# Optimization experiments

Hardware: AMD Instinct MI355X
Metric: run time of the kernel (lower is better)

Reference implementation:

```python
import jax, jax.numpy as jnp
import numpy as np

RATIO = 0.25
RADIUS = 0.2
K = 32  # PyG radius() default max_num_neighbors


def fps(pos, n_samples):
    """Farthest point sampling for one cloud. pos: [N,3] -> indices [S]."""
    d2 = jnp.sum((pos - pos[0]) ** 2, axis=-1)  # dist to first (deterministic start)
    idx0 = jnp.zeros((n_samples,), jnp.int32)

    def body(i, state):
        idx, d = state
        nxt = jnp.argmax(d).astype(jnp.int32)
        idx = idx.at[i].set(nxt)
        d = jnp.minimum(d, jnp.sum((pos - pos[nxt]) ** 2, axis=-1))
        return idx, d

    idx, _ = jax.lax.fori_loop(1, n_samples, body, (idx0, d2))
    return idx


def setup_inputs() -> dict:
    key = jax.random.key(0)
    k0, k1, k2, k3 = jax.random.split(key, 4)
    B, N, C = 16, 4096, 64
    x = jax.random.normal(k0, (B, N, C), jnp.float32)
    pos = jax.random.uniform(k1, (B, N, 3), jnp.float32)  # unit cube
    W1 = jax.random.normal(k2, (C + 3, 128), jnp.float32) / np.sqrt(C + 3).astype(np.float32)
    b1 = jnp.zeros((128,), jnp.float32)
    W2 = jax.random.normal(k3, (128, 256), jnp.float32) / np.sqrt(128).astype(np.float32)
    b2 = jnp.zeros((256,), jnp.float32)
    return {"x": x, "pos": pos, "W1": W1, "b1": b1, "W2": W2, "b2": b2}


def reference(x, pos, W1, b1, W2, b2):
    B, N, C = x.shape
    S = int(N * RATIO)
    r2 = RADIUS * RADIUS

    # --- FPS per cloud ---
    samp = jax.vmap(lambda p: fps(p, S))(pos)            # [B,S] int32
    pos_s = jnp.take_along_axis(pos, samp[..., None], axis=1)  # [B,S,3]

    # --- ball query: K nearest within radius of each centroid ---
    d2 = jnp.sum((pos_s[:, :, None, :] - pos[:, None, :, :]) ** 2, axis=-1)  # [B,S,N]
    neg = jnp.where(d2 <= r2, -d2, -jnp.inf)
    negk, nbr = jax.lax.top_k(neg, K)                    # [B,S,K]
    valid = negk > -jnp.inf                              # centroid itself (d2=0) always valid

    # --- gather -> local MLP -> max pool (PointConv with max aggregation) ---
    x_j = jax.vmap(lambda xb, nb: xb[nb])(x, nbr)        # [B,S,K,C]
    pos_j = jax.vmap(lambda pb, nb: pb[nb])(pos, nbr)    # [B,S,K,3]
    rel = pos_j - pos_s[:, :, None, :]                   # pos_j - pos_i
    h = jnp.concatenate([x_j, rel], axis=-1)             # [B,S,K,C+3]
    h = jax.nn.relu(jnp.einsum("bskc,cd->bskd", h, W1) + b1)
    h = jax.nn.relu(jnp.einsum("bskd,de->bske", h, W2) + b2)
    h = jnp.where(valid[..., None], h, -jnp.inf)
    out = jnp.max(h, axis=2)                             # [B,S,256]
    return out, pos_s
```

## Files before the change

kernel.cpp:

```cpp
#include <hip/hip_runtime.h>
#include <stdint.h>

typedef unsigned short u16;
typedef unsigned int u32;
typedef unsigned long long u64;

#define NB 16
#define NP 4096
#define NCH 64
#define NS 1024
#define NK 32
#define H1D 128
#define H2D 256
#define KP1 96
#define LDA 104
#define LDH 136
#define OUTOFF (NB * NS * H2D)

typedef __attribute__((ext_vector_type(8))) short bfrag;
typedef __attribute__((ext_vector_type(4))) float facc4;
typedef __attribute__((ext_vector_type(2))) float f32x2;

__device__ __forceinline__ u16 f2bf(float f) {
  u32 u = __float_as_uint(f);
  u += 0x7FFFu + ((u >> 16) & 1u);
  return (u16)(u >> 16);
}

__device__ __forceinline__ float dist2(float ax, float ay, float az,
                                       float bx, float by, float bz) {
#pragma clang fp contract(off)
  float dx = ax - bx, dy = ay - by, dz = az - bz;
  return dx * dx + dy * dy + dz * dz;
}

__device__ __forceinline__ f32x2 dist2v(f32x2 ax, f32x2 ay, f32x2 az,
                                        float bx, float by, float bz) {
#pragma clang fp contract(off)
  f32x2 dx = ax - bx, dy = ay - by, dz = az - bz;
  return dx * dx + dy * dy + dz * dz;
}

__device__ __forceinline__ float wave_max_f32(float v) {
  const int NI = (int)0xFF800000u;
  v = fmaxf(v, __int_as_float(__builtin_amdgcn_update_dpp(NI, __float_as_int(v), 0x111, 0xf, 0xf, false)));
  v = fmaxf(v, __int_as_float(__builtin_amdgcn_update_dpp(NI, __float_as_int(v), 0x112, 0xf, 0xf, false)));
  v = fmaxf(v, __int_as_float(__builtin_amdgcn_update_dpp(NI, __float_as_int(v), 0x114, 0xf, 0xf, false)));
  v = fmaxf(v, __int_as_float(__builtin_amdgcn_update_dpp(NI, __float_as_int(v), 0x118, 0xf, 0xf, false)));
  v = fmaxf(v, __int_as_float(__builtin_amdgcn_update_dpp(NI, __float_as_int(v), 0x142, 0xa, 0xf, false)));
  v = fmaxf(v, __int_as_float(__builtin_amdgcn_update_dpp(NI, __float_as_int(v), 0x143, 0xc, 0xf, false)));
  return __int_as_float(__builtin_amdgcn_readlane(__float_as_int(v), 63));
}

__device__ __forceinline__ u32 wave_min_u32(u32 v) {
  u32 t;
  t = (u32)__builtin_amdgcn_update_dpp(-1, (int)v, 0x111, 0xf, 0xf, false); v = t < v ? t : v;
  t = (u32)__builtin_amdgcn_update_dpp(-1, (int)v, 0x112, 0xf, 0xf, false); v = t < v ? t : v;
  t = (u32)__builtin_amdgcn_update_dpp(-1, (int)v, 0x114, 0xf, 0xf, false); v = t < v ? t : v;
  t = (u32)__builtin_amdgcn_update_dpp(-1, (int)v, 0x118, 0xf, 0xf, false); v = t < v ? t : v;
  t = (u32)__builtin_amdgcn_update_dpp(-1, (int)v, 0x142, 0xa, 0xf, false); v = t < v ? t : v;
  t = (u32)__builtin_amdgcn_update_dpp(-1, (int)v, 0x143, 0xc, 0xf, false); v = t < v ? t : v;
  return (u32)__builtin_amdgcn_readlane((int)v, 63);
}

#define QUAD_MAX_STEP(CTRL)                                                           \
  {                                                                                   \
    const u32 plo = (u32)__builtin_amdgcn_update_dpp(0, (int)klo, (CTRL), 0xf, 0xf, true); \
    const u32 phi = (u32)__builtin_amdgcn_update_dpp(0, (int)khi, (CTRL), 0xf, 0xf, true); \
    const u32 pqx = (u32)__builtin_amdgcn_update_dpp(0, (int)qxu, (CTRL), 0xf, 0xf, true); \
    const u32 pqy = (u32)__builtin_amdgcn_update_dpp(0, (int)qyu, (CTRL), 0xf, 0xf, true); \
    const u32 pqz = (u32)__builtin_amdgcn_update_dpp(0, (int)qzu, (CTRL), 0xf, 0xf, true); \
    const u64 ok = ((u64)phi << 32) | plo;                                            \
    const u64 mk = ((u64)khi << 32) | klo;                                            \
    if (ok > mk) { klo = plo; khi = phi; qxu = pqx; qyu = pqy; qzu = pqz; }           \
  }

__global__ void setup_kernel(const float* __restrict__ W1, const float* __restrict__ W2,
                             u16* __restrict__ W1T, u16* __restrict__ W2T) {
  int idx = blockIdx.x * 256 + threadIdx.x;
  if (idx < H1D * KP1) {
    int n = idx / KP1, k = idx % KP1;
    W1T[idx] = f2bf(k < 67 ? W1[k * H1D + n] : 0.f);
  } else if (idx < H1D * KP1 + H2D * H1D) {
    int j = idx - H1D * KP1;
    int n = j / H1D, k = j % H1D;
    W2T[j] = f2bf(W2[k * H2D + n]);
  }
}

__global__ __launch_bounds__(256) void fps_kernel(const float* __restrict__ pos,
                                                  int* __restrict__ samp,
                                                  float* __restrict__ pos_s) {
  __shared__ float4 plds[NP];
  __shared__ __align__(16) u32 recs[2][4][8];
  const int b = blockIdx.x;
  const int tid = threadIdx.x;
  const int lane = tid & 63, wv = tid >> 6;
  const float* pb = pos + (size_t)b * NP * 3;
  for (int k = tid; k < NP; k += 256)
    plds[k] = make_float4(pb[k * 3 + 0], pb[k * 3 + 1], pb[k * 3 + 2], 0.f);
  __syncthreads();

  f32x2 px2[8], py2[8], pz2[8], dd[8];
  const float4 q0 = plds[0];
  float bv = -1.f;
  int bj = 0;
#pragma unroll
  for (int t = 0; t < 8; ++t) {
    const float4 pA = plds[tid * 16 + 2 * t];
    const float4 pB = plds[tid * 16 + 2 * t + 1];
    px2[t] = (f32x2){pA.x, pB.x};
    py2[t] = (f32x2){pA.y, pB.y};
    pz2[t] = (f32x2){pA.z, pB.z};
    const f32x2 s = dist2v(px2[t], py2[t], pz2[t], q0.x, q0.y, q0.z);
    dd[t] = s;
    const bool c0 = s.x > bv; bv = c0 ? s.x : bv; bj = c0 ? 2 * t : bj;
    const bool c1 = s.y > bv; bv = c1 ? s.y : bv; bj = c1 ? 2 * t + 1 : bj;
  }
  if (tid == 0) {
    samp[b * NS] = 0;
    pos_s[(size_t)b * NS * 3 + 0] = q0.x;
    pos_s[(size_t)b * NS * 3 + 1] = q0.y;
    pos_s[(size_t)b * NS * 3 + 2] = q0.z;
  }

  for (int i = 1; i < NS; ++i) {
    const int gidx = tid * 16 + bj;
    const float4 cpos = plds[gidx];
    const float wmax = wave_max_f32(bv);
    const u64 mask = __ballot(bv == wmax);
    const bool winner = (bv == wmax) && ((mask & ((1ull << lane) - 1ull)) == 0ull);
    if (winner) {
      u32* rp = &recs[i & 1][wv][0];
      *(uint4*)rp = make_uint4(4095u - (u32)gidx, __float_as_uint(bv),
                               __float_as_uint(cpos.x), __float_as_uint(cpos.y));
      rp[4] = __float_as_uint(cpos.z);
    }
    __syncthreads();
    const u32* sp = &recs[i & 1][lane & 3][0];
    const uint4 rA = *(const uint4*)sp;
    u32 klo = rA.x, khi = rA.y, qxu = rA.z, qyu = rA.w, qzu = sp[4];
    QUAD_MAX_STEP(0xB1)
    QUAD_MAX_STEP(0x4E)
    const float qx = __uint_as_float(qxu);
    const float qy = __uint_as_float(qyu);
    const float qz = __uint_as_float(qzu);
    if (tid == 0) {
      samp[b * NS + i] = 4095 - (int)(klo & 0xFFFu);
      pos_s[((size_t)b * NS + i) * 3 + 0] = qx;
      pos_s[((size_t)b * NS + i) * 3 + 1] = qy;
      pos_s[((size_t)b * NS + i) * 3 + 2] = qz;
    }
    bv = -1.f; bj = 0;
#pragma unroll
    for (int t = 0; t < 8; ++t) {
      const f32x2 s = dist2v(px2[t], py2[t], pz2[t], qx, qy, qz);
      dd[t].x = fminf(dd[t].x, s.x);
      dd[t].y = fminf(dd[t].y, s.y);
      const bool c0 = dd[t].x > bv; bv = c0 ? dd[t].x : bv; bj = c0 ? 2 * t : bj;
      const bool c1 = dd[t].y > bv; bv = c1 ? dd[t].y : bv; bj = c1 ? 2 * t + 1 : bj;
    }
  }
}

__global__ __launch_bounds__(256) void ballq_kernel(const float* __restrict__ pos,
                                                    const int* __restrict__ samp,
                                                    int* __restrict__ nbr) {
  __shared__ u64 buf[4][256];
  const int lane = threadIdx.x & 63, wv = threadIdx.x >> 6;
  const int sg = blockIdx.x * 4 + wv;
  const int b = sg >> 10;
  const int nc = samp[sg];
  const float* pb = pos + (size_t)b * NP * 3;
  const float cx = pb[nc * 3 + 0], cy = pb[nc * 3 + 1], cz = pb[nc * 3 + 2];
  const float r2 = (float)(0.2 * 0.2);
  int V = 0;
  for (int c = 0; c < 64; ++c) {
    const int i = c * 64 + lane;
    const float d2v = dist2(cx, cy, cz, pb[i * 3 + 0], pb[i * 3 + 1], pb[i * 3 + 2]);
    const bool valid = d2v <= r2;
    const u64 bal = __ballot(valid);
    if (valid) {
      const int rank = __popcll(bal & ((1ull << lane) - 1ull));
      const int p = V + rank;
      if (p < 256) buf[wv][p] = ((u64)__float_as_uint(d2v) << 32) | (u32)i;
    }
    V += __popcll(bal);
  }
  if (V > 256) V = 256;
  u32 kd[4], ki[4];
#pragma unroll
  for (int t = 0; t < 4; ++t) {
    const int p = t * 64 + lane;
    const u64 v = (p < V) ? buf[wv][p] : ~0ull;
    kd[t] = (u32)(v >> 32);
    ki[t] = (u32)v;
  }
  u32 my = 0, pad = 0;
  for (int e = 0; e < 32; ++e) {
    u32 m0 = kd[0] < kd[1] ? kd[0] : kd[1];
    u32 m1 = kd[2] < kd[3] ? kd[2] : kd[3];
    const u32 m = wave_min_u32(m0 < m1 ? m0 : m1);
    u32 ci = 0xFFFFFFFFu;
#pragma unroll
    for (int t = 0; t < 4; ++t) {
      const u32 cm = (ki[t] < ci) ? ki[t] : ci;
      ci = (kd[t] == m) ? cm : ci;
    }
    const u32 wi = wave_min_u32(ci);
    if (e == 0) pad = wi;
    const u32 sel = (m == 0xFFFFFFFFu) ? pad : wi;
    if (lane == e) my = sel;
#pragma unroll
    for (int t = 0; t < 4; ++t)
      if (ki[t] == wi) kd[t] = 0xFFFFFFFFu;
  }
  if (lane < 32) nbr[(size_t)sg * NK + lane] = (int)my;
}

__global__ __launch_bounds__(256) void mlp_kernel(
    const float* __restrict__ x, const float* __restrict__ pos,
    const float* __restrict__ b1, const float* __restrict__ b2,
    const int* __restrict__ nbr, const u16* __restrict__ W1T,
    const u16* __restrict__ W2T, const float* __restrict__ pos_s,
    float* __restrict__ out) {
  __shared__ u16 A[128 * LDA];
  __shared__ u16 Hs[128 * LDH];
  const int ctr0 = blockIdx.x * 4;
  const int b = ctr0 >> 10;
  const int tid = threadIdx.x;
  {
    const int row = tid >> 1, half = tid & 1;
    const int g = ctr0 + (row >> 5);
    const int n = nbr[(size_t)g * NK + (row & 31)];
    const float4* xr = (const float4*)(x + ((size_t)b * NP + n) * NCH + half * 32);
#pragma unroll
    for (int qq = 0; qq < 4; ++qq) {
      const float4 v0 = xr[2 * qq], v1 = xr[2 * qq + 1];
      uint4 wp;
      wp.x = (u32)f2bf(v0.x) | ((u32)f2bf(v0.y) << 16);
      wp.y = (u32)f2bf(v0.z) | ((u32)f2bf(v0.w) << 16);
      wp.z = (u32)f2bf(v1.x) | ((u32)f2bf(v1.y) << 16);
      wp.w = (u32)f2bf(v1.z) | ((u32)f2bf(v1.w) << 16);
      *(uint4*)&A[row * LDA + half * 32 + qq * 8] = wp;
    }
    if (half == 0) {
      const float rx = pos[((size_t)b * NP + n) * 3 + 0] - pos_s[(size_t)g * 3 + 0];
      const float ry = pos[((size_t)b * NP + n) * 3 + 1] - pos_s[(size_t)g * 3 + 1];
      const float rz = pos[((size_t)b * NP + n) * 3 + 2] - pos_s[(size_t)g * 3 + 2];
      uint4 wr;
      wr.x = (u32)f2bf(rx) | ((u32)f2bf(ry) << 16);
      wr.y = (u32)f2bf(rz);
      wr.z = 0; wr.w = 0;
      uint4 wz;
      wz.x = wz.y = wz.z = wz.w = 0;
      *(uint4*)&A[row * LDA + 64] = wr;
      *(uint4*)&A[row * LDA + 72] = wz;
      *(uint4*)&A[row * LDA + 80] = wz;
      *(uint4*)&A[row * LDA + 88] = wz;
    }
  }
  __syncthreads();
  const int lane = tid & 63, w = tid >> 6;
  const int r16 = lane & 15, g4 = lane >> 4;
  {
    bfrag af[2][3];
#pragma unroll
    for (int mg2 = 0; mg2 < 2; ++mg2)
#pragma unroll
      for (int ks = 0; ks < 3; ++ks)
        af[mg2][ks] = *(const bfrag*)&A[((2 * w + mg2) * 16 + r16) * LDA + ks * 32 + g4 * 8];
#pragma unroll
    for (int ng = 0; ng < 8; ++ng) {
      const bfrag bw0 = *(const bfrag*)&W1T[(ng * 16 + r16) * KP1 + 0 + g4 * 8];
      const bfrag bw1 = *(const bfrag*)&W1T[(ng * 16 + r16) * KP1 + 32 + g4 * 8];
      const bfrag bw2 = *(const bfrag*)&W1T[(ng * 16 + r16) * KP1 + 64 + g4 * 8];
      facc4 a0 = {0.f, 0.f, 0.f, 0.f}, a1 = {0.f, 0.f, 0.f, 0.f};
      a0 = __builtin_amdgcn_mfma_f32_16x16x32_bf16(bw0, af[0][0], a0, 0, 0, 0);
      a0 = __builtin_amdgcn_mfma_f32_16x16x32_bf16(bw1, af[0][1], a0, 0, 0, 0);
      a0 = __builtin_amdgcn_mfma_f32_16x16x32_bf16(bw2, af[0][2], a0, 0, 0, 0);
      a1 = __builtin_amdgcn_mfma_f32_16x16x32_bf16(bw0, af[1][0], a1, 0, 0, 0);
      a1 = __builtin_amdgcn_mfma_f32_16x16x32_bf16(bw1, af[1][1], a1, 0, 0, 0);
      a1 = __builtin_amdgcn_mfma_f32_16x16x32_bf16(bw2, af[1][2], a1, 0, 0, 0);
      const float4 bias4 = *(const float4*)&b1[ng * 16 + g4 * 4];
      const int nb = ng * 16 + g4 * 4;
      u32 lo0 = (u32)f2bf(fmaxf(a0[0] + bias4.x, 0.f)) | ((u32)f2bf(fmaxf(a0[1] + bias4.y, 0.f)) << 16);
      u32 hi0 = (u32)f2bf(fmaxf(a0[2] + bias4.z, 0.f)) | ((u32)f2bf(fmaxf(a0[3] + bias4.w, 0.f)) << 16);
      u32 lo1 = (u32)f2bf(fmaxf(a1[0] + bias4.x, 0.f)) | ((u32)f2bf(fmaxf(a1[1] + bias4.y, 0.f)) << 16);
      u32 hi1 = (u32)f2bf(fmaxf(a1[2] + bias4.z, 0.f)) | ((u32)f2bf(fmaxf(a1[3] + bias4.w, 0.f)) << 16);
      *(uint2*)&Hs[((2 * w + 0) * 16 + r16) * LDH + nb] = make_uint2(lo0, hi0);
      *(uint2*)&Hs[((2 * w + 1) * 16 + r16) * LDH + nb] = make_uint2(lo1, hi1);
    }
  }
  __syncthreads();
  {
    bfrag hf[2][4];
#pragma unroll
    for (int mg2 = 0; mg2 < 2; ++mg2)
#pragma unroll
      for (int ks = 0; ks < 4; ++ks)
        hf[mg2][ks] = *(const bfrag*)&Hs[((2 * w + mg2) * 16 + r16) * LDH + ks * 32 + g4 * 8];
    const int gout = ctr0 + w;
    const int NI = (int)0xFF800000u;
#pragma unroll
    for (int ng = 0; ng < 16; ++ng) {
      facc4 a0 = {0.f, 0.f, 0.f, 0.f}, a1 = {0.f, 0.f, 0.f, 0.f};
#pragma unroll
      for (int ks = 0; ks < 4; ++ks) {
        const bfrag bw = *(const bfrag*)&W2T[(ng * 16 + r16) * H1D + ks * 32 + g4 * 8];
        a0 = __builtin_amdgcn_mfma_f32_16x16x32_bf16(bw, hf[0][ks], a0, 0, 0, 0);
        a1 = __builtin_amdgcn_mfma_f32_16x16x32_bf16(bw, hf[1][ks], a1, 0, 0, 0);
      }
      float v0 = fmaxf(a0[0], a1[0]);
      float v1 = fmaxf(a0[1], a1[1]);
      float v2 = fmaxf(a0[2], a1[2]);
      float v3 = fmaxf(a0[3], a1[3]);
      v0 = fmaxf(v0, __int_as_float(__builtin_amdgcn_update_dpp(NI, __float_as_int(v0), 0x111, 0xf, 0xf, false)));
      v1 = fmaxf(v1, __int_as_float(__builtin_amdgcn_update_dpp(NI, __float_as_int(v1), 0x111, 0xf, 0xf, false)));
      v2 = fmaxf(v2, __int_as_float(__builtin_amdgcn_update_dpp(NI, __float_as_int(v2), 0x111, 0xf, 0xf, false)));
      v3 = fmaxf(v3, __int_as_float(__builtin_amdgcn_update_dpp(NI, __float_as_int(v3), 0x111, 0xf, 0xf, false)));
      v0 = fmaxf(v0, __int_as_float(__builtin_amdgcn_update_dpp(NI, __float_as_int(v0), 0x112, 0xf, 0xf, false)));
      v1 = fmaxf(v1, __int_as_float(__builtin_amdgcn_update_dpp(NI, __float_as_int(v1), 0x112, 0xf, 0xf, false)));
      v2 = fmaxf(v2, __int_as_float(__builtin_amdgcn_update_dpp(NI, __float_as_int(v2), 0x112, 0xf, 0xf, false)));
      v3 = fmaxf(v3, __int_as_float(__builtin_amdgcn_update_dpp(NI, __float_as_int(v3), 0x112, 0xf, 0xf, false)));
      v0 = fmaxf(v0, __int_as_float(__builtin_amdgcn_update_dpp(NI, __float_as_int(v0), 0x114, 0xf, 0xf, false)));
      v1 = fmaxf(v1, __int_as_float(__builtin_amdgcn_update_dpp(NI, __float_as_int(v1), 0x114, 0xf, 0xf, false)));
      v2 = fmaxf(v2, __int_as_float(__builtin_amdgcn_update_dpp(NI, __float_as_int(v2), 0x114, 0xf, 0xf, false)));
      v3 = fmaxf(v3, __int_as_float(__builtin_amdgcn_update_dpp(NI, __float_as_int(v3), 0x114, 0xf, 0xf, false)));
      v0 = fmaxf(v0, __int_as_float(__builtin_amdgcn_update_dpp(NI, __float_as_int(v0), 0x118, 0xf, 0xf, false)));
      v1 = fmaxf(v1, __int_as_float(__builtin_amdgcn_update_dpp(NI, __float_as_int(v1), 0x118, 0xf, 0xf, false)));
      v2 = fmaxf(v2, __int_as_float(__builtin_amdgcn_update_dpp(NI, __float_as_int(v2), 0x118, 0xf, 0xf, false)));
      v3 = fmaxf(v3, __int_as_float(__builtin_amdgcn_update_dpp(NI, __float_as_int(v3), 0x118, 0xf, 0xf, false)));
      if ((lane & 15) == 15) {
        const float4 b24 = *(const float4*)&b2[ng * 16 + g4 * 4];
        float4 o;
        o.x = fmaxf(v0 + b24.x, 0.f);
        o.y = fmaxf(v1 + b24.y, 0.f);
        o.z = fmaxf(v2 + b24.z, 0.f);
        o.w = fmaxf(v3 + b24.w, 0.f);
        *(float4*)&out[(size_t)gout * H2D + ng * 16 + g4 * 4] = o;
      }
    }
  }
}

extern "C" void kernel_launch(void* const* d_in, const int* in_sizes, int n_in,
                              void* d_out, int out_size, void* d_ws, size_t ws_size,
                              hipStream_t stream) {
  const float* x = (const float*)d_in[0];
  const float* pos = (const float*)d_in[1];
  const float* W1 = (const float*)d_in[2];
  const float* b1 = (const float*)d_in[3];
  const float* W2 = (const float*)d_in[4];
  const float* b2 = (const float*)d_in[5];
  float* out = (float*)d_out;
  char* ws = (char*)d_ws;
  u16* W1T = (u16*)(ws + 0);
  u16* W2T = (u16*)(ws + 24576);
  int* samp = (int*)(ws + 90112);
  int* nbr = (int*)(ws + 155648);
  float* pos_s = out + OUTOFF;

  setup_kernel<<<dim3(176), dim3(256), 0, stream>>>(W1, W2, W1T, W2T);
  fps_kernel<<<dim3(NB), dim3(256), 0, stream>>>(pos, samp, pos_s);
  ballq_kernel<<<dim3(NB * NS / 4), dim3(256), 0, stream>>>(pos, samp, nbr);
  mlp_kernel<<<dim3(NB * NS / 4), dim3(256), 0, stream>>>(x, pos, b1, b2, nbr, W1T, W2T,
                                                          pos_s, out);
}
```

Measured before the change: 917.8 us.

## Fuse FPS, ball query and MLP into persistent producer-consumer kernel

Three kernels are merged into one persistent launch. Sixteen blocks run FPS per cloud and publish progress counters with release atomics. The other 240 blocks spin on those counters and run ball query plus the two-layer MLP on groups of 8 centroids as soon as they are sampled. The goal is to hide the serial FPS latency behind the neighbour search and MLP work, and to avoid the nbr round trip through global memory. In exchange it relies on all 256 blocks being co-resident, uses spin-wait polling, and adds a spare wave in each FPS block to write the results.

New measurement: 1.062 ms. +15.7%, slower.

```diff
diff --git a/kernel.cpp b/kernel.cpp
--- a/kernel.cpp
+++ b/kernel.cpp
@@ -16,6 +16,8 @@
 #define LDA 104
 #define LDH 136
 #define OUTOFF (NB * NS * H2D)
+#define NCONS 240
+#define NGRP 2048
 
 typedef __attribute__((ext_vector_type(8))) short bfrag;
 typedef __attribute__((ext_vector_type(4))) float facc4;
@@ -88,258 +90,290 @@
   }
 }
 
-__global__ __launch_bounds__(256) void fps_kernel(const float* __restrict__ pos,
-                                                  int* __restrict__ samp,
-                                                  float* __restrict__ pos_s) {
-  __shared__ float4 plds[NP];
-  __shared__ __align__(16) u32 recs[2][4][8];
-  const int b = blockIdx.x;
+__global__ __launch_bounds__(512) void fused_kernel(
+    const float* __restrict__ x, const float* __restrict__ pos,
+    const float* __restrict__ b1, const float* __restrict__ b2,
+    const u16* __restrict__ W1T, const u16* __restrict__ W2T,
+    int* __restrict__ samp, u32* __restrict__ prog, float* __restrict__ out) {
+  __shared__ __align__(16) unsigned char smem[123936];
   const int tid = threadIdx.x;
-  const int lane = tid & 63, wv = tid >> 6;
-  const float* pb = pos + (size_t)b * NP * 3;
-  for (int k = tid; k < NP; k += 256)
-    plds[k] = make_float4(pb[k * 3 + 0], pb[k * 3 + 1], pb[k * 3 + 2], 0.f);
-  __syncthreads();
-
-  f32x2 px2[8], py2[8], pz2[8], dd[8];
-  const float4 q0 = plds[0];
-  float bv = -1.f;
-  int bj = 0;
-#pragma unroll
-  for (int t = 0; t < 8; ++t) {
-    const float4 pA = plds[tid * 16 + 2 * t];
-    const float4 pB = plds[tid * 16 + 2 * t + 1];
-    px2[t] = (f32x2){pA.x, pB.x};
-    py2[t] = (f32x2){pA.y, pB.y};
-    pz2[t] = (f32x2){pA.z, pB.z};
-    const f32x2 s = dist2v(px2[t], py2[t], pz2[t], q0.x, q0.y, q0.z);
-    dd[t] = s;
-    const bool c0 = s.x > bv; bv = c0 ? s.x : bv; bj = c0 ? 2 * t : bj;
-    const bool c1 = s.y > bv; bv = c1 ? s.y : bv; bj = c1 ? 2 * t + 1 : bj;
-  }
-  if (tid == 0) {
-    samp[b * NS] = 0;
-    pos_s[(size_t)b * NS * 3 + 0] = q0.x;
-    pos_s[(size_t)b * NS * 3 + 1] = q0.y;
-    pos_s[(size_t)b * NS * 3 + 2] = q0.z;
-  }
-
-  for (int i = 1; i < NS; ++i) {
-    const int gidx = tid * 16 + bj;
-    const float4 cpos = plds[gidx];
-    const float wmax = wave_max_f32(bv);
-    const u64 mask = __ballot(bv == wmax);
-    const bool winner = (bv == wmax) && ((mask & ((1ull << lane) - 1ull)) == 0ull);
-    if (winner) {
-      u32* rp = &recs[i & 1][wv][0];
-      *(uint4*)rp = make_uint4(4095u - (u32)gidx, __float_as_uint(bv),
-                               __float_as_uint(cpos.x), __float_as_uint(cpos.y));
-      rp[4] = __float_as_uint(cpos.z);
+  const int lane = tid & 63, w = tid >> 6;
+
+  if (blockIdx.x < 16) {
+    float4* plds = (float4*)smem;
+    u32* recs = (u32*)(smem + 65536);
+    float* pos_s = out + OUTOFF;
+    const int b = blockIdx.x;
+    const float* pb = pos + (size_t)b * NP * 3;
+    for (int k = tid; k < NP; k += 512)
+      plds[k] = make_float4(pb[k * 3 + 0], pb[k * 3 + 1], pb[k * 3 + 2], 0.f);
+    __syncthreads();
+
+    f32x2 px2[8], py2[8], pz2[8], dd[8];
+    float bv = -1.f;
+    int bj = 0;
+    if (tid < 256) {
+      const float4 q0 = plds[0];
+#pragma unroll
+      for (int t = 0; t < 8; ++t) {
+        const float4 pA = plds[tid * 16 + 2 * t];
+        const float4 pB = plds[tid * 16 + 2 * t + 1];
+        px2[t] = (f32x2){pA.x, pB.x};
+        py2[t] = (f32x2){pA.y, pB.y};
+        pz2[t] = (f32x2){pA.z, pB.z};
+        const f32x2 s = dist2v(px2[t], py2[t], pz2[t], q0.x, q0.y, q0.z);
+        dd[t] = s;
+        const bool c0 = s.x > bv; bv = c0 ? s.x : bv; bj = c0 ? 2 * t : bj;
+        const bool c1 = s.y > bv; bv = c1 ? s.y : bv; bj = c1 ? 2 * t + 1 : bj;
+      }
+      if (tid == 0) {
+        pos_s[(size_t)b * NS * 3 + 0] = q0.x;
+        pos_s[(size_t)b * NS * 3 + 1] = q0.y;
+        pos_s[(size_t)b * NS * 3 + 2] = q0.z;
+      }
+    } else if (tid == 256) {
+      __hip_atomic_store(&samp[b * NS], 0, __ATOMIC_RELAXED, __HIP_MEMORY_SCOPE_AGENT);
+    }
+    for (int i = 1; i < NS; ++i) {
+      if (tid < 256) {
+        const int gidx = tid * 16 + bj;
+        const float4 cpos = plds[gidx];
+        const float wmax = wave_max_f32(bv);
+        const u64 mask = __ballot(bv == wmax);
+        const bool winner = (bv == wmax) && ((mask & ((1ull << lane) - 1ull)) == 0ull);
+        if (winner) {
+          u32* rp = &recs[(((i & 1) << 2) + w) * 8];
+          *(uint4*)rp = make_uint4(4095u - (u32)gidx, __float_as_uint(bv),
+                                   __float_as_uint(cpos.x), __float_as_uint(cpos.y));
+          rp[4] = __float_as_uint(cpos.z);
+        }
+      }
+      __syncthreads();
+      if (tid < 256) {
+        const u32* sp = &recs[(((i & 1) << 2) + (lane & 3)) * 8];
+        const uint4 rA = *(const uint4*)sp;
+        u32 klo = rA.x, khi = rA.y, qxu = rA.z, qyu = rA.w, qzu = sp[4];
+        QUAD_MAX_STEP(0xB1)
+        QUAD_MAX_STEP(0x4E)
+        const float qx = __uint_as_float(qxu);
+        const float qy = __uint_as_float(qyu);
+        const float qz = __uint_as_float(qzu);
+        bv = -1.f; bj = 0;
+#pragma unroll
+        for (int t = 0; t < 8; ++t) {
+          const f32x2 s = dist2v(px2[t], py2[t], pz2[t], qx, qy, qz);
+          dd[t].x = fminf(dd[t].x, s.x);
+          dd[t].y = fminf(dd[t].y, s.y);
+          const bool c0 = dd[t].x > bv; bv = c0 ? dd[t].x : bv; bj = c0 ? 2 * t : bj;
+          const bool c1 = dd[t].y > bv; bv = c1 ? dd[t].y : bv; bj = c1 ? 2 * t + 1 : bj;
+        }
+      } else if (w == 4) {
+        const u32* sp = &recs[(((i & 1) << 2) + (lane & 3)) * 8];
+        const uint4 rA = *(const uint4*)sp;
+        u32 klo = rA.x, khi = rA.y, qxu = rA.z, qyu = rA.w, qzu = sp[4];
+        QUAD_MAX_STEP(0xB1)
+        QUAD_MAX_STEP(0x4E)
+        if (lane == 0) {
+          const int gi = 4095 - (int)(klo & 0xFFFu);
+          __hip_atomic_store(&samp[b * NS + i], gi, __ATOMIC_RELAXED,
+                             __HIP_MEMORY_SCOPE_AGENT);
+          pos_s[((size_t)b * NS + i) * 3 + 0] = __uint_as_float(qxu);
+          pos_s[((size_t)b * NS + i) * 3 + 1] = __uint_as_float(qyu);
+          pos_s[((size_t)b * NS + i) * 3 + 2] = __uint_as_float(qzu);
+          if ((i & 15) == 0) {
+            __hip_atomic_store(&prog[b], (u32)i, __ATOMIC_RELEASE,
+                               __HIP_MEMORY_SCOPE_AGENT);
+          }
+        }
+      }
     }
     __syncthreads();
-    const u32* sp = &recs[i & 1][lane & 3][0];
-    const uint4 rA = *(const uint4*)sp;
-    u32 klo = rA.x, khi = rA.y, qxu = rA.z, qyu = rA.w, qzu = sp[4];
-    QUAD_MAX_STEP(0xB1)
-    QUAD_MAX_STEP(0x4E)
-    const float qx = __uint_as_float(qxu);
-    const float qy = __uint_as_float(qyu);
-    const float qz = __uint_as_float(qzu);
-    if (tid == 0) {
-      samp[b * NS + i] = 4095 - (int)(klo & 0xFFFu);
-      pos_s[((size_t)b * NS + i) * 3 + 0] = qx;
-      pos_s[((size_t)b * NS + i) * 3 + 1] = qy;
-      pos_s[((size_t)b * NS + i) * 3 + 2] = qz;
+    if (tid == 256) {
+      __hip_atomic_store(&prog[b], (u32)NS, __ATOMIC_RELEASE,
+                         __HIP_MEMORY_SCOPE_AGENT);
     }
-    bv = -1.f; bj = 0;
-#pragma unroll
-    for (int t = 0; t < 8; ++t) {
-      const f32x2 s = dist2v(px2[t], py2[t], pz2[t], qx, qy, qz);
-      dd[t].x = fminf(dd[t].x, s.x);
-      dd[t].y = fminf(dd[t].y, s.y);
-      const bool c0 = dd[t].x > bv; bv = c0 ? dd[t].x : bv; bj = c0 ? 2 * t : bj;
-      const bool c1 = dd[t].y > bv; bv = c1 ? dd[t].y : bv; bj = c1 ? 2 * t + 1 : bj;
-    }
-  }
-}
-
-__global__ __launch_bounds__(256) void ballq_kernel(const float* __restrict__ pos,
-                                                    const int* __restrict__ samp,
-                                                    int* __restrict__ nbr) {
-  __shared__ u64 buf[4][256];
-  const int lane = threadIdx.x & 63, wv = threadIdx.x >> 6;
-  const int sg = blockIdx.x * 4 + wv;
-  const int b = sg >> 10;
-  const int nc = samp[sg];
-  const float* pb = pos + (size_t)b * NP * 3;
-  const float cx = pb[nc * 3 + 0], cy = pb[nc * 3 + 1], cz = pb[nc * 3 + 2];
-  const float r2 = (float)(0.2 * 0.2);
-  int V = 0;
-  for (int c = 0; c < 64; ++c) {
-    const int i = c * 64 + lane;
-    const float d2v = dist2(cx, cy, cz, pb[i * 3 + 0], pb[i * 3 + 1], pb[i * 3 + 2]);
-    const bool valid = d2v <= r2;
-    const u64 bal = __ballot(valid);
-    if (valid) {
-      const int rank = __popcll(bal & ((1ull << lane) - 1ull));
-      const int p = V + rank;
-      if (p < 256) buf[wv][p] = ((u64)__float_as_uint(d2v) << 32) | (u32)i;
-    }
-    V += __popcll(bal);
-  }
-  if (V > 256) V = 256;
-  u32 kd[4], ki[4];
-#pragma unroll
-  for (int t = 0; t < 4; ++t) {
-    const int p = t * 64 + lane;
-    const u64 v = (p < V) ? buf[wv][p] : ~0ull;
-    kd[t] = (u32)(v >> 32);
-    ki[t] = (u32)v;
-  }
-  u32 my = 0, pad = 0;
-  for (int e = 0; e < 32; ++e) {
-    u32 m0 = kd[0] < kd[1] ? kd[0] : kd[1];
-    u32 m1 = kd[2] < kd[3] ? kd[2] : kd[3];
-    const u32 m = wave_min_u32(m0 < m1 ? m0 : m1);
-    u32 ci = 0xFFFFFFFFu;
-#pragma unroll
-    for (int t = 0; t < 4; ++t) {
-      const u32 cm = (ki[t] < ci) ? ki[t] : ci;
-      ci = (kd[t] == m) ? cm : ci;
-    }
-    const u32 wi = wave_min_u32(ci);
-    if (e == 0) pad = wi;
-    const u32 sel = (m == 0xFFFFFFFFu) ? pad : wi;
-    if (lane == e) my = sel;
-#pragma unroll
-    for (int t = 0; t < 4; ++t)
-      if (ki[t] == wi) kd[t] = 0xFFFFFFFFu;
-  }
-  if (lane < 32) nbr[(size_t)sg * NK + lane] = (int)my;
-}
-
-__global__ __launch_bounds__(256) void mlp_kernel(
-    const float* __restrict__ x, const float* __restrict__ pos,
-    const float* __restrict__ b1, const float* __restrict__ b2,
-    const int* __restrict__ nbr, const u16* __restrict__ W1T,
-    const u16* __restrict__ W2T, const float* __restrict__ pos_s,
-    float* __restrict__ out) {
-  __shared__ u16 A[128 * LDA];
-  __shared__ u16 Hs[128 * LDH];
-  const int ctr0 = blockIdx.x * 4;
-  const int b = ctr0 >> 10;
-  const int tid = threadIdx.x;
-  {
-    const int row = tid >> 1, half = tid & 1;
-    const int g = ctr0 + (row >> 5);
-    const int n = nbr[(size_t)g * NK + (row & 31)];
-    const float4* xr = (const float4*)(x + ((size_t)b * NP + n) * NCH + half * 32);
-#pragma unroll
-    for (int qq = 0; qq < 4; ++qq) {
-      const float4 v0 = xr[2 * qq], v1 = xr[2 * qq + 1];
-      uint4 wp;
-      wp.x = (u32)f2bf(v0.x) | ((u32)f2bf(v0.y) << 16);
-      wp.y = (u32)f2bf(v0.z) | ((u32)f2bf(v0.w) << 16);
-      wp.z = (u32)f2bf(v1.x) | ((u32)f2bf(v1.y) << 16);
-      wp.w = (u32)f2bf(v1.z) | ((u32)f2bf(v1.w) << 16);
-      *(uint4*)&A[row * LDA + half * 32 + qq * 8] = wp;
-    }
-    if (half == 0) {
-      const float rx = pos[((size_t)b * NP + n) * 3 + 0] - pos_s[(size_t)g * 3 + 0];
-      const float ry = pos[((size_t)b * NP + n) * 3 + 1] - pos_s[(size_t)g * 3 + 1];
-      const float rz = pos[((size_t)b * NP + n) * 3 + 2] - pos_s[(size_t)g * 3 + 2];
-      uint4 wr;
-      wr.x = (u32)f2bf(rx) | ((u32)f2bf(ry) << 16);
-      wr.y = (u32)f2bf(rz);
-      wr.z = 0; wr.w = 0;
-      uint4 wz;
-      wz.x = wz.y = wz.z = wz.w = 0;
-      *(uint4*)&A[row * LDA + 64] = wr;
-      *(uint4*)&A[row * LDA + 72] = wz;
-      *(uint4*)&A[row * LDA + 80] = wz;
-      *(uint4*)&A[row * LDA + 88] = wz;
-    }
-  }
-  __syncthreads();
-  const int lane = tid & 63, w = tid >> 6;
-  const int r16 = lane & 15, g4 = lane >> 4;
-  {
-    bfrag af[2][3];
-#pragma unroll
-    for (int mg2 = 0; mg2 < 2; ++mg2)
-#pragma unroll
-      for (int ks = 0; ks < 3; ++ks)
-        af[mg2][ks] = *(const bfrag*)&A[((2 * w + mg2) * 16 + r16) * LDA + ks * 32 + g4 * 8];
-#pragma unroll
-    for (int ng = 0; ng < 8; ++ng) {
-      const bfrag bw0 = *(const bfrag*)&W1T[(ng * 16 + r16) * KP1 + 0 + g4 * 8];
-      const bfrag bw1 = *(const bfrag*)&W1T[(ng * 16 + r16) * KP1 + 32 + g4 * 8];
-      const bfrag bw2 = *(const bfrag*)&W1T[(ng * 16 + r16) * KP1 + 64 + g4 * 8];
-      facc4 a0 = {0.f, 0.f, 0.f, 0.f}, a1 = {0.f, 0.f, 0.f, 0.f};
-      a0 = __builtin_amdgcn_mfma_f32_16x16x32_bf16(bw0, af[0][0], a0, 0, 0, 0);
-      a0 = __builtin_amdgcn_mfma_f32_16x16x32_bf16(bw1, af[0][1], a0, 0, 0, 0);
-      a0 = __builtin_amdgcn_mfma_f32_16x16x32_bf16(bw2, af[0][2], a0, 0, 0, 0);
-      a1 = __builtin_amdgcn_mfma_f32_16x16x32_bf16(bw0, af[1][0], a1, 0, 0, 0);
-      a1 = __builtin_amdgcn_mfma_f32_16x16x32_bf16(bw1, af[1][1], a1, 0, 0, 0);
-      a1 = __builtin_amdgcn_mfma_f32_16x16x32_bf16(bw2, af[1][2], a1, 0, 0, 0);
-      const float4 bias4 = *(const float4*)&b1[ng * 16 + g4 * 4];
-      const int nb = ng * 16 + g4 * 4;
-      u32 lo0 = (u32)f2bf(fmaxf(a0[0] + bias4.x, 0.f)) | ((u32)f2bf(fmaxf(a0[1] + bias4.y, 0.f)) << 16);
-      u32 hi0 = (u32)f2bf(fmaxf(a0[2] + bias4.z, 0.f)) | ((u32)f2bf(fmaxf(a0[3] + bias4.w, 0.f)) << 16);
-      u32 lo1 = (u32)f2bf(fmaxf(a1[0] + bias4.x, 0.f)) | ((u32)f2bf(fmaxf(a1[1] + bias4.y, 0.f)) << 16);
-      u32 hi1 = (u32)f2bf(fmaxf(a1[2] + bias4.z, 0.f)) | ((u32)f2bf(fmaxf(a1[3] + bias4.w, 0.f)) << 16);
-      *(uint2*)&Hs[((2 * w + 0) * 16 + r16) * LDH + nb] = make_uint2(lo0, hi0);
-      *(uint2*)&Hs[((2 * w + 1) * 16 + r16) * LDH + nb] = make_uint2(lo1, hi1);
-    }
-  }
-  __syncthreads();
-  {
-    bfrag hf[2][4];
-#pragma unroll
-    for (int mg2 = 0; mg2 < 2; ++mg2)
-#pragma unroll
-      for (int ks = 0; ks < 4; ++ks)
-        hf[mg2][ks] = *(const bfrag*)&Hs[((2 * w + mg2) * 16 + r16) * LDH + ks * 32 + g4 * 8];
-    const int gout = ctr0 + w;
-    const int NI = (int)0xFF800000u;
-#pragma unroll
-    for (int ng = 0; ng < 16; ++ng) {
-      facc4 a0 = {0.f, 0.f, 0.f, 0.f}, a1 = {0.f, 0.f, 0.f, 0.f};
-#pragma unroll
-      for (int ks = 0; ks < 4; ++ks) {
-        const bfrag bw = *(const bfrag*)&W2T[(ng * 16 + r16) * H1D + ks * 32 + g4 * 8];
-        a0 = __builtin_amdgcn_mfma_f32_16x16x32_bf16(bw, hf[0][ks], a0, 0, 0, 0);
-        a1 = __builtin_amdgcn_mfma_f32_16x16x32_bf16(bw, hf[1][ks], a1, 0, 0, 0);
-      }
-      float v0 = fmaxf(a0[0], a1[0]);
-      float v1 = fmaxf(a0[1], a1[1]);
-      float v2 = fmaxf(a0[2], a1[2]);
-      float v3 = fmaxf(a0[3], a1[3]);
-      v0 = fmaxf(v0, __int_as_float(__builtin_amdgcn_update_dpp(NI, __float_as_int(v0), 0x111, 0xf, 0xf, false)));
-      v1 = fmaxf(v1, __int_as_float(__builtin_amdgcn_update_dpp(NI, __float_as_int(v1), 0x111, 0xf, 0xf, false)));
-      v2 = fmaxf(v2, __int_as_float(__builtin_amdgcn_update_dpp(NI, __float_as_int(v2), 0x111, 0xf, 0xf, false)));
-      v3 = fmaxf(v3, __int_as_float(__builtin_amdgcn_update_dpp(NI, __float_as_int(v3), 0x111, 0xf, 0xf, false)));
-      v0 = fmaxf(v0, __int_as_float(__builtin_amdgcn_update_dpp(NI, __float_as_int(v0), 0x112, 0xf, 0xf, false)));
-      v1 = fmaxf(v1, __int_as_float(__builtin_amdgcn_update_dpp(NI, __float_as_int(v1), 0x112, 0xf, 0xf, false)));
-      v2 = fmaxf(v2, __int_as_float(__builtin_amdgcn_update_dpp(NI, __float_as_int(v2), 0x112, 0xf, 0xf, false)));
-      v3 = fmaxf(v3, __int_as_float(__builtin_amdgcn_update_dpp(NI, __float_as_int(v3), 0x112, 0xf, 0xf, false)));
-      v0 = fmaxf(v0, __int_as_float(__builtin_amdgcn_update_dpp(NI, __float_as_int(v0), 0x114, 0xf, 0xf, false)));
-      v1 = fmaxf(v1, __int_as_float(__builtin_amdgcn_update_dpp(NI, __float_as_int(v1), 0x114, 0xf, 0xf, false)));
-      v2 = fmaxf(v2, __int_as_float(__builtin_amdgcn_update_dpp(NI, __float_as_int(v2), 0x114, 0xf, 0xf, false)));
-      v3 = fmaxf(v3, __int_as_float(__builtin_amdgcn_update_dpp(NI, __float_as_int(v3), 0x114, 0xf, 0xf, false)));
-      v0 = fmaxf(v0, __int_as_float(__builtin_amdgcn_update_dpp(NI, __float_as_int(v0), 0x118, 0xf, 0xf, false)));
-      v1 = fmaxf(v1, __int_as_float(__builtin_amdgcn_update_dpp(NI, __float_as_int(v1), 0x118, 0xf, 0xf, false)));
-      v2 = fmaxf(v2, __int_as_float(__builtin_amdgcn_update_dpp(NI, __float_as_int(v2), 0x118, 0xf, 0xf, false)));
-      v3 = fmaxf(v3, __int_as_float(__builtin_amdgcn_update_dpp(NI, __float_as_int(v3), 0x118, 0xf, 0xf, false)));
-      if ((lane & 15) == 15) {
-        const float4 b24 = *(const float4*)&b2[ng * 16 + g4 * 4];
-        float4 o;
-        o.x = fmaxf(v0 + b24.x, 0.f);
-        o.y = fmaxf(v1 + b24.y, 0.f);
-        o.z = fmaxf(v2 + b24.z, 0.f);
-        o.w = fmaxf(v3 + b24.w, 0.f);
-        *(float4*)&out[(size_t)gout * H2D + ng * 16 + g4 * 4] = o;
-      }
+  } else {
+    u64* qbuf = (u64*)smem;
+    u16* A = (u16*)smem;
+    u16* Hs = (u16*)(smem + 53248);
+    int* s_nbr = (int*)(smem + 122880);
+    int* s_nc = (int*)(smem + 123904);
+    const int r16 = lane & 15, g4 = lane >> 4;
+    for (int G = (int)blockIdx.x - 16; G < NGRP; G += NCONS) {
+      const int b = G & 15;
+      const int i0 = (G >> 4) << 3;
+      if (tid == 0) {
+        const u32 need = (u32)(i0 + 8);
+        while (__hip_atomic_load(&prog[b], __ATOMIC_ACQUIRE,
+                                 __HIP_MEMORY_SCOPE_AGENT) < need)
+          __builtin_amdgcn_s_sleep(32);
+      }
+      __syncthreads();
+      if (tid < 8)
+        s_nc[tid] = __hip_atomic_load(&samp[b * NS + i0 + tid], __ATOMIC_RELAXED,
+                                      __HIP_MEMORY_SCOPE_AGENT);
+      __syncthreads();
+      const float* pb = pos + (size_t)b * NP * 3;
+      {
+        const int nc = s_nc[w];
+        const float cx = pb[nc * 3 + 0], cy = pb[nc * 3 + 1], cz = pb[nc * 3 + 2];
+        const float r2 = (float)(0.2 * 0.2);
+        u64* qb = qbuf + (size_t)w * 256;
+        int V = 0;
+        for (int c = 0; c < 64; ++c) {
+          const int i = c * 64 + lane;
+          const float d2v = dist2(cx, cy, cz, pb[i * 3 + 0], pb[i * 3 + 1], pb[i * 3 + 2]);
+          const bool valid = d2v <= r2;
+          const u64 bal = __ballot(valid);
+          if (valid) {
+            const int rank = __popcll(bal & ((1ull << lane) - 1ull));
+            const int p = V + rank;
+            if (p < 256) qb[p] = ((u64)__float_as_uint(d2v) << 32) | (u32)i;
+          }
+          V += __popcll(bal);
+        }
+        if (V > 256) V = 256;
+        u32 kd[4], ki[4];
+#pragma unroll
+        for (int t = 0; t < 4; ++t) {
+          const int p = t * 64 + lane;
+          const u64 v = (p < V) ? qb[p] : ~0ull;
+          kd[t] = (u32)(v >> 32);
+          ki[t] = (u32)v;
+        }
+        u32 my = 0, pad = 0;
+        for (int e = 0; e < 32; ++e) {
+          u32 m0 = kd[0] < kd[1] ? kd[0] : kd[1];
+          u32 m1 = kd[2] < kd[3] ? kd[2] : kd[3];
+          const u32 m = wave_min_u32(m0 < m1 ? m0 : m1);
+          u32 ci = 0xFFFFFFFFu;
+#pragma unroll
+          for (int t = 0; t < 4; ++t) {
+            const u32 cm = (ki[t] < ci) ? ki[t] : ci;
+            ci = (kd[t] == m) ? cm : ci;
+          }
+          const u32 wi = wave_min_u32(ci);
+          if (e == 0) pad = wi;
+          const u32 sel = (m == 0xFFFFFFFFu) ? pad : wi;
+          if (lane == e) my = sel;
+#pragma unroll
+          for (int t = 0; t < 4; ++t)
+            if (ki[t] == wi) kd[t] = 0xFFFFFFFFu;
+        }
+        if (lane < 32) s_nbr[w * 32 + lane] = (int)my;
+      }
+      __syncthreads();
+      {
+        const int row = tid >> 1, half = tid & 1;
+        const int n = s_nbr[(row >> 5) * 32 + (row & 31)];
+        const float4* xr = (const float4*)(x + ((size_t)b * NP + n) * NCH + half * 32);
+#pragma unroll
+        for (int qq = 0; qq < 4; ++qq) {
+          const float4 v0 = xr[2 * qq], v1 = xr[2 * qq + 1];
+          uint4 wp;
+          wp.x = (u32)f2bf(v0.x) | ((u32)f2bf(v0.y) << 16);
+          wp.y = (u32)f2bf(v0.z) | ((u32)f2bf(v0.w) << 16);
+          wp.z = (u32)f2bf(v1.x) | ((u32)f2bf(v1.y) << 16);
+          wp.w = (u32)f2bf(v1.z) | ((u32)f2bf(v1.w) << 16);
+          *(uint4*)&A[row * LDA + half * 32 + qq * 8] = wp;
+        }
+        if (half == 0) {
+          const int ncg = s_nc[row >> 5];
+          const float rx = pb[n * 3 + 0] - pb[ncg * 3 + 0];
+          const float ry = pb[n * 3 + 1] - pb[ncg * 3 + 1];
+          const float rz = pb[n * 3 + 2] - pb[ncg * 3 + 2];
+          uint4 wr;
+          wr.x = (u32)f2bf(rx) | ((u32)f2bf(ry) << 16);
+          wr.y = (u32)f2bf(rz);
+          wr.z = 0; wr.w = 0;
+          uint4 wz; wz.x = wz.y = wz.z = wz.w = 0;
+          *(uint4*)&A[row * LDA + 64] = wr;
+          *(uint4*)&A[row * LDA + 72] = wz;
+          *(uint4*)&A[row * LDA + 80] = wz;
+          *(uint4*)&A[row * LDA + 88] = wz;
+        }
+      }
+      __syncthreads();
+      {
+        bfrag af[2][3];
+#pragma unroll
+        for (int mg2 = 0; mg2 < 2; ++mg2)
+#pragma unroll
+          for (int ks = 0; ks < 3; ++ks)
+            af[mg2][ks] = *(const bfrag*)&A[((2 * w + mg2) * 16 + r16) * LDA + ks * 32 + g4 * 8];
+#pragma unroll
+        for (int ng = 0; ng < 8; ++ng) {
+          const bfrag bw0 = *(const bfrag*)&W1T[(ng * 16 + r16) * KP1 + 0 + g4 * 8];
+          const bfrag bw1 = *(const bfrag*)&W1T[(ng * 16 + r16) * KP1 + 32 + g4 * 8];
+          const bfrag bw2 = *(const bfrag*)&W1T[(ng * 16 + r16) * KP1 + 64 + g4 * 8];
+          facc4 a0 = {0.f, 0.f, 0.f, 0.f}, a1 = {0.f, 0.f, 0.f, 0.f};
+          a0 = __builtin_amdgcn_mfma_f32_16x16x32_bf16(bw0, af[0][0], a0, 0, 0, 0);
+          a0 = __builtin_amdgcn_mfma_f32_16x16x32_bf16(bw1, af[0][1], a0, 0, 0, 0);
+          a0 = __builtin_amdgcn_mfma_f32_16x16x32_bf16(bw2, af[0][2], a0, 0, 0, 0);
+          a1 = __builtin_amdgcn_mfma_f32_16x16x32_bf16(bw0, af[1][0], a1, 0, 0, 0);
+          a1 = __builtin_amdgcn_mfma_f32_16x16x32_bf16(bw1, af[1][1], a1, 0, 0, 0);
+          a1 = __builtin_amdgcn_mfma_f32_16x16x32_bf16(bw2, af[1][2], a1, 0, 0, 0);
+          const float4 bias4 = *(const float4*)&b1[ng * 16 + g4 * 4];
+          const int nb = ng * 16 + g4 * 4;
+          u32 lo0 = (u32)f2bf(fmaxf(a0[0] + bias4.x, 0.f)) | ((u32)f2bf(fmaxf(a0[1] + bias4.y, 0.f)) << 16);
+          u32 hi0 = (u32)f2bf(fmaxf(a0[2] + bias4.z, 0.f)) | ((u32)f2bf(fmaxf(a0[3] + bias4.w, 0.f)) << 16);
+          u32 lo1 = (u32)f2bf(fmaxf(a1[0] + bias4.x, 0.f)) | ((u32)f2bf(fmaxf(a1[1] + bias4.y, 0.f)) << 16);
+          u32 hi1 = (u32)f2bf(fmaxf(a1[2] + bias4.z, 0.f)) | ((u32)f2bf(fmaxf(a1[3] + bias4.w, 0.f)) << 16);
+          *(uint2*)&Hs[((2 * w + 0) * 16 + r16) * LDH + nb] = make_uint2(lo0, hi0);
+          *(uint2*)&Hs[((2 * w + 1) * 16 + r16) * LDH + nb] = make_uint2(lo1, hi1);
+        }
+      }
+      __syncthreads();
+      {
+        bfrag hf[2][4];
+#pragma unroll
+        for (int mg2 = 0; mg2 < 2; ++mg2)
+#pragma unroll
+          for (int ks = 0; ks < 4; ++ks)
+            hf[mg2][ks] = *(const bfrag*)&Hs[((2 * w + mg2) * 16 + r16) * LDH + ks * 32 + g4 * 8];
+        const size_t gout = (size_t)(b * NS + i0 + w);
+        const int NI = (int)0xFF800000u;
+#pragma unroll
+        for (int ng = 0; ng < 16; ++ng) {
+          facc4 a0 = {0.f, 0.f, 0.f, 0.f}, a1 = {0.f, 0.f, 0.f, 0.f};
+#pragma unroll
+          for (int ks = 0; ks < 4; ++ks) {
+            const bfrag bw = *(const bfrag*)&W2T[(ng * 16 + r16) * H1D + ks * 32 + g4 * 8];
+            a0 = __builtin_amdgcn_mfma_f32_16x16x32_bf16(bw, hf[0][ks], a0, 0, 0, 0);
+            a1 = __builtin_amdgcn_mfma_f32_16x16x32_bf16(bw, hf[1][ks], a1, 0, 0, 0);
+          }
+          float v0 = fmaxf(a0[0], a1[0]);
+          float v1 = fmaxf(a0[1], a1[1]);
+          float v2 = fmaxf(a0[2], a1[2]);
+          float v3 = fmaxf(a0[3], a1[3]);
+          v0 = fmaxf(v0, __int_as_float(__builtin_amdgcn_update_dpp(NI, __float_as_int(v0), 0x111, 0xf, 0xf, false)));
+          v1 = fmaxf(v1, __int_as_float(__builtin_amdgcn_update_dpp(NI, __float_as_int(v1), 0x111, 0xf, 0xf, false)));
+          v2 = fmaxf(v2, __int_as_float(__builtin_amdgcn_update_dpp(NI, __float_as_int(v2), 0x111, 0xf, 0xf, false)));
+          v3 = fmaxf(v3, __int_as_float(__builtin_amdgcn_update_dpp(NI, __float_as_int(v3), 0x111, 0xf, 0xf, false)));
+          v0 = fmaxf(v0, __int_as_float(__builtin_amdgcn_update_dpp(NI, __float_as_int(v0), 0x112, 0xf, 0xf, false)));
+          v1 = fmaxf(v1, __int_as_float(__builtin_amdgcn_update_dpp(NI, __float_as_int(v1), 0x112, 0xf, 0xf, false)));
+          v2 = fmaxf(v2, __int_as_float(__builtin_amdgcn_update_dpp(NI, __float_as_int(v2), 0x112, 0xf, 0xf, false)));
+          v3 = fmaxf(v3, __int_as_float(__builtin_amdgcn_update_dpp(NI, __float_as_int(v3), 0x112, 0xf, 0xf, false)));
+          v0 = fmaxf(v0, __int_as_float(__builtin_amdgcn_update_dpp(NI, __float_as_int(v0), 0x114, 0xf, 0xf, false)));
+          v1 = fmaxf(v1, __int_as_float(__builtin_amdgcn_update_dpp(NI, __float_as_int(v1), 0x114, 0xf, 0xf, false)));
+          v2 = fmaxf(v2, __int_as_float(__builtin_amdgcn_update_dpp(NI, __float_as_int(v2), 0x114, 0xf, 0xf, false)));
+          v3 = fmaxf(v3, __int_as_float(__builtin_amdgcn_update_dpp(NI, __float_as_int(v3), 0x114, 0xf, 0xf, false)));
+          v0 = fmaxf(v0, __int_as_float(__builtin_amdgcn_update_dpp(NI, __float_as_int(v0), 0x118, 0xf, 0xf, false)));
+          v1 = fmaxf(v1, __int_as_float(__builtin_amdgcn_update_dpp(NI, __float_as_int(v1), 0x118, 0xf, 0xf, false)));
+          v2 = fmaxf(v2, __int_as_float(__builtin_amdgcn_update_dpp(NI, __float_as_int(v2), 0x118, 0xf, 0xf, false)));
+          v3 = fmaxf(v3, __int_as_float(__builtin_amdgcn_update_dpp(NI, __float_as_int(v3), 0x118, 0xf, 0xf, false)));
+          if ((lane & 15) == 15) {
+            const float4 b24 = *(const float4*)&b2[ng * 16 + g4 * 4];
+            float4 o;
+            o.x = fmaxf(v0 + b24.x, 0.f);
+            o.y = fmaxf(v1 + b24.y, 0.f);
+            o.z = fmaxf(v2 + b24.z, 0.f);
+            o.w = fmaxf(v3 + b24.w, 0.f);
+            *(float4*)&out[gout * H2D + ng * 16 + g4 * 4] = o;
+          }
+        }
+      }
+      __syncthreads();
     }
   }
 }
@@ -358,12 +392,10 @@
   u16* W1T = (u16*)(ws + 0);
   u16* W2T = (u16*)(ws + 24576);
   int* samp = (int*)(ws + 90112);
-  int* nbr = (int*)(ws + 155648);
-  float* pos_s = out + OUTOFF;
-
+  u32* prog = (u32*)(ws + 155648);
+
+  hipMemsetAsync(ws + 155648, 0, 64, stream);
   setup_kernel<<<dim3(176), dim3(256), 0, stream>>>(W1, W2, W1T, W2T);
-  fps_kernel<<<dim3(NB), dim3(256), 0, stream>>>(pos, samp, pos_s);
-  ballq_kernel<<<dim3(NB * NS / 4), dim3(256), 0, stream>>>(pos, samp, nbr);
-  mlp_kernel<<<dim3(NB * NS / 4), dim3(256), 0, stream>>>(x, pos, b1, b2, nbr, W1T, W2T,
-                                                          pos_s, out);
-}
+  fused_kernel<<<dim3(256), dim3(512), 0, stream>>>(x, pos, b1, b2, W1T, W2T, samp,
+                                                    prog, out);
+}
```
